# Kernel tuning notes

Measured on AMD Instinct MI355X. Metric: run time of the kernel, lower is better.

Reference implementation:

```python
import jax, jax.numpy as jnp
import numpy as np

EMBED_DIM = 1024
NUM_HEADS = 16
HEAD_DIM = EMBED_DIM // NUM_HEADS


def setup_inputs() -> dict:
    key = jax.random.key(0)
    k_x, k_wqkv, k_bqkv, k_wo, k_bo = jax.random.split(key, 5)
    b, n = 2, 2048
    scale_in = 1.0 / np.sqrt(EMBED_DIM)
    return {
        "x": jax.random.normal(k_x, (b, n, EMBED_DIM), dtype=jnp.float32),
        "W_qkv": jax.random.normal(k_wqkv, (EMBED_DIM, 3 * EMBED_DIM), dtype=jnp.float32) * scale_in,
        "b_qkv": jnp.zeros((3 * EMBED_DIM,), dtype=jnp.float32),
        "W_out": jax.random.normal(k_wo, (EMBED_DIM, EMBED_DIM), dtype=jnp.float32) * scale_in,
        "b_out": jnp.zeros((EMBED_DIM,), dtype=jnp.float32),
    }


def _rope_rotate(t, cos, sin):
    # t: [b, h, n, hd]; cos/sin: [1, 1, n, hd//2]
    t1, t2 = jnp.split(t, 2, axis=-1)
    return jnp.concatenate([cos * t1 - sin * t2, sin * t1 + cos * t2], axis=-1)


def reference(x, W_qkv, b_qkv, W_out, b_out):
    b, n, d = x.shape
    h, hd = NUM_HEADS, HEAD_DIM

    qkv = x @ W_qkv + b_qkv                      # [b, n, 3d]
    q, k, v = jnp.split(qkv, 3, axis=-1)
    q, k, v = [t.reshape(b, n, h, hd).transpose(0, 2, 1, 3) for t in (q, k, v)]

    # RoPE tables
    hd2 = hd // 2
    theta = 10000.0 ** (-2.0 * jnp.arange(hd2, dtype=jnp.float32) / hd)
    freqs = jnp.arange(n, dtype=jnp.float32)[:, None] * theta[None, :]  # [n, hd2]
    cos = jnp.cos(freqs)[None, None]
    sin = jnp.sin(freqs)[None, None]
    q = _rope_rotate(q, cos, sin)
    k = _rope_rotate(k, cos, sin)

    scores = jnp.einsum('bhqd,bhkd->bhqk', q, k) / jnp.sqrt(jnp.float32(hd))
    attn = jax.nn.softmax(scores, axis=-1)       # [b, h, n, n]
    out = jnp.einsum('bhqk,bhkd->bhqd', attn, v)
    out = out.transpose(0, 2, 1, 3).reshape(b, n, d)
    return out @ W_out + b_out
```

## Files before the change

### kernel.cpp

```cpp
#include <hip/hip_runtime.h>
#include <hip/hip_bf16.h>
#include <math.h>

#define EMBED 1024
#define NHEAD 16
#define HD 64
#define BATCH 2
#define SEQ 2048
#define MTOT (BATCH * SEQ)
#define QKVN (3 * EMBED)

typedef __attribute__((ext_vector_type(8))) short short8;
typedef __attribute__((ext_vector_type(4))) float f32x4;

typedef __attribute__((address_space(1))) const unsigned int GUI;
typedef __attribute__((address_space(3))) unsigned int LUI;

__device__ __forceinline__ void gload_lds16(const void* src, void* dst) {
  __builtin_amdgcn_global_load_lds((GUI*)src, (LUI*)dst, 16, 0, 0);
}

__device__ __forceinline__ unsigned short f2bf(float f) {
  unsigned u = __builtin_bit_cast(unsigned, f);
  u += 0x7fffu + ((u >> 16) & 1u);
  return (unsigned short)(u >> 16);
}

__device__ __forceinline__ unsigned cvt_pk_bf16(float lo, float hi) {
  unsigned r;
  asm("v_cvt_pk_bf16_f32 %0, %1, %2" : "=v"(r) : "v"(lo), "v"(hi));
  return r;
}


__global__ __launch_bounds__(256) void k_cvt(const float* __restrict__ in,
                                             unsigned short* __restrict__ out, int n4) {
  int i = blockIdx.x * 256 + threadIdx.x;
  if (i >= n4) return;
  float4 v = reinterpret_cast<const float4*>(in)[i];
  ushort4 o;
  o.x = f2bf(v.x); o.y = f2bf(v.y); o.z = f2bf(v.z); o.w = f2bf(v.w);
  reinterpret_cast<ushort4*>(out)[i] = o;
}

__global__ __launch_bounds__(256) void k_transpose_cvt(const float* __restrict__ W,
                                                       unsigned short* __restrict__ WT,
                                                       int K, int Ncols) {
  __shared__ float tile[32][33];
  int n0 = blockIdx.x * 32, k0 = blockIdx.y * 32;
  int tc = threadIdx.x & 31, tr = threadIdx.x >> 5;
  for (int i = 0; i < 4; i++) {
    int r = tr + i * 8;
    tile[r][tc] = W[(size_t)(k0 + r) * Ncols + n0 + tc];
  }
  __syncthreads();
  for (int i = 0; i < 4; i++) {
    int r = tr + i * 8;
    WT[(size_t)(n0 + r) * K + k0 + tc] = f2bf(tile[tc][r]);
  }
}

__global__ __launch_bounds__(256) void k_rope_tables(float* __restrict__ cosT,
                                                     float* __restrict__ sinT) {
  int idx = blockIdx.x * 256 + threadIdx.x;
  if (idx >= SEQ * 32) return;
  int pos = idx >> 5, i = idx & 31;
  double theta = exp((double)i * -0.28782313662425575);
  double f = (double)pos * theta;
  cosT[idx] = (float)cos(f);
  sinT[idx] = (float)sin(f);
}

__device__ __forceinline__ void gemm_mainloop(const unsigned short* __restrict__ A,
                                              const unsigned short* __restrict__ Bt,
                                              unsigned short* Al, unsigned short* Bl,
                                              size_t m0, size_t n0,
                                              int tid, int l15, int g, int wm, int wn,
                                              f32x4 acc[4][4]) {
  const int w = tid >> 6;
  const int lane = tid & 63;
  const int srow = lane >> 3, slot = lane & 7;
  for (int k0 = 0; k0 < 1024; k0 += 64) {
    __syncthreads();
    for (int it = 0; it < 4; it++) {
      const int r = w * 32 + it * 8 + srow;
      const int sc = (slot ^ (r & 7)) * 8;
      gload_lds16(A + (m0 + r) * 1024 + k0 + sc, &Al[(w * 32 + it * 8) * 64]);
      gload_lds16(Bt + (n0 + r) * 1024 + k0 + sc, &Bl[(w * 32 + it * 8) * 64]);
    }
    __syncthreads();
    for (int kk = 0; kk < 2; kk++) {
      short8 fa[4], fb[4];
      const int xr = ((kk * 4 + g) ^ (l15 & 7)) * 8;
      for (int i = 0; i < 4; i++)
        fa[i] = *reinterpret_cast<const short8*>(&Al[(wm * 64 + i * 16 + l15) * 64 + xr]);
      for (int j = 0; j < 4; j++)
        fb[j] = *reinterpret_cast<const short8*>(&Bl[(wn * 64 + j * 16 + l15) * 64 + xr]);
      for (int i = 0; i < 4; i++)
        for (int j = 0; j < 4; j++)
          acc[i][j] = __builtin_amdgcn_mfma_f32_16x16x32_bf16(fa[i], fb[j], acc[i][j], 0, 0, 0);
    }
  }
}

__global__ __launch_bounds__(256) void k_qkv_gemm(const unsigned short* __restrict__ A,
                                                  const unsigned short* __restrict__ Bt,
                                                  const float* __restrict__ bias,
                                                  const float* __restrict__ cosT,
                                                  const float* __restrict__ sinT,
                                                  unsigned short* __restrict__ Qb,
                                                  unsigned short* __restrict__ Kb,
                                                  unsigned short* __restrict__ Vtg) {
  __shared__ alignas(16) unsigned short Al[128 * 64];
  __shared__ alignas(16) unsigned short Bl[128 * 64];
  const int tid = threadIdx.x;
  const int lane = tid & 63, l15 = lane & 15, g = lane >> 4;
  const int wid = tid >> 6, wm = wid >> 1, wn = wid & 1;
  const size_t m0 = (size_t)blockIdx.y * 128;
  const size_t n0 = (size_t)blockIdx.x * 128;
  f32x4 acc[4][4] = {};
  gemm_mainloop(A, Bt, Al, Bl, m0, n0, tid, l15, g, wm, wn, acc);

  const int cbase = (int)n0 + wn * 64;
  const int sec = cbase >> 10;
  const int head = (cbase & 1023) >> 6;
  float bia[4];
  for (int j = 0; j < 4; j++) bia[j] = bias[cbase + j * 16 + l15];
  const size_t mw = m0 + wm * 64;

  if (sec == 2) {
    for (int i = 0; i < 4; i++)
      for (int r = 0; r < 4; r++) {
        size_t m = mw + i * 16 + g * 4 + r;
        int bb = (int)(m >> 11), pos = (int)(m & 2047);
        size_t hb = (size_t)(bb * NHEAD + head) * HD;
        for (int j = 0; j < 4; j++) {
          int d = j * 16 + l15;
          Vtg[(hb + d) * SEQ + pos] = f2bf(acc[i][j][r] + bia[j]);
        }
      }
  } else {
    unsigned short* dst = sec ? Kb : Qb;
    const float qs = sec ? 1.0f : 0.125f;
    for (int i = 0; i < 4; i++)
      for (int r = 0; r < 4; r++) {
        size_t m = mw + i * 16 + g * 4 + r;
        int bb = (int)(m >> 11), pos = (int)(m & 2047);
        size_t base = ((size_t)(bb * NHEAD + head) * SEQ + pos) * HD;
        const float* cr = cosT + pos * 32;
        const float* sr = sinT + pos * 32;
        for (int pl = 0; pl < 2; pl++) {
          int ii = pl * 16 + l15;
          float c = cr[ii], s = sr[ii];
          float lo = acc[i][pl][r] + bia[pl];
          float hi = acc[i][pl + 2][r] + bia[pl + 2];
          dst[base + ii]      = f2bf((c * lo - s * hi) * qs);
          dst[base + 32 + ii] = f2bf((s * lo + c * hi) * qs);
        }
      }
  }
}

__global__ __launch_bounds__(256) void k_out_gemm(const unsigned short* __restrict__ A,
                                                  const unsigned short* __restrict__ Bt,
                                                  const float* __restrict__ bias,
                                                  float* __restrict__ out) {
  __shared__ alignas(16) unsigned short Al[128 * 64];
  __shared__ alignas(16) unsigned short Bl[128 * 64];
  const int tid = threadIdx.x;
  const int lane = tid & 63, l15 = lane & 15, g = lane >> 4;
  const int wid = tid >> 6, wm = wid >> 1, wn = wid & 1;
  const size_t m0 = (size_t)blockIdx.y * 128;
  const size_t n0 = (size_t)blockIdx.x * 128;
  f32x4 acc[4][4] = {};
  gemm_mainloop(A, Bt, Al, Bl, m0, n0, tid, l15, g, wm, wn, acc);

  const int cbase = (int)n0 + wn * 64;
  const size_t mw = m0 + wm * 64;
  for (int i = 0; i < 4; i++)
    for (int r = 0; r < 4; r++) {
      size_t m = mw + i * 16 + g * 4 + r;
      for (int j = 0; j < 4; j++) {
        int col = cbase + j * 16 + l15;
        out[m * EMBED + col] = acc[i][j][r] + bias[col];
      }
    }
}

__global__ __launch_bounds__(256) void k_attn(const unsigned short* __restrict__ Q,
                                              const unsigned short* __restrict__ Kg,
                                              const unsigned short* __restrict__ Vtg,
                                              unsigned short* __restrict__ AO) {
  __shared__ alignas(16) unsigned short Kt[64 * 64];
  __shared__ alignas(16) unsigned short Vt[64 * 64];
  const int tid = threadIdx.x, w = tid >> 6, lane = tid & 63;
  const int l15 = lane & 15, g = lane >> 4;
  const int srow = lane >> 3, slot = lane & 7;
  const int bh = blockIdx.y;
  const unsigned short* Qp = Q + (size_t)bh * SEQ * HD;
  const unsigned short* Kp = Kg + (size_t)bh * SEQ * HD;
  const unsigned short* Vp = Vtg + (size_t)bh * HD * SEQ;
  const int q0 = blockIdx.x * 64 + w * 16;

  short8 aq[2];
  for (int kk = 0; kk < 2; kk++)
    aq[kk] = *reinterpret_cast<const short8*>(Qp + (size_t)(q0 + l15) * HD + kk * 32 + g * 8);

  f32x4 o[4] = {};
  float mrow = -INFINITY, lrow = 0.f;

  for (int t = 0; t < SEQ / 64; t++) {
    const int kb = t * 64;
    __syncthreads();
    for (int it = 0; it < 2; it++) {
      const int r = w * 16 + it * 8 + srow;
      const int sc = (slot ^ (r & 7)) * 8;
      gload_lds16(Kp + (size_t)(kb + r) * HD + sc, &Kt[(w * 16 + it * 8) * 64]);
      gload_lds16(Vp + (size_t)r * SEQ + kb + sc, &Vt[(w * 16 + it * 8) * 64]);
    }
    __syncthreads();

    f32x4 s[4] = {};
    for (int kk = 0; kk < 2; kk++) {
      const int xr = ((kk * 4 + g) ^ (l15 & 7)) * 8;
      for (int c = 0; c < 4; c++) {
        short8 ak = *reinterpret_cast<const short8*>(&Kt[(c * 16 + l15) * 64 + xr]);
        s[c] = __builtin_amdgcn_mfma_f32_16x16x32_bf16(ak, aq[kk], s[c], 0, 0, 0);
      }
    }

    float tm = s[0][0];
#pragma unroll
    for (int c = 0; c < 4; c++)
#pragma unroll
      for (int r = 0; r < 4; r++) tm = fmaxf(tm, s[c][r]);
    tm = fmaxf(tm, __shfl_xor(tm, 16, 64));
    tm = fmaxf(tm, __shfl_xor(tm, 32, 64));

    if (!__all(tm <= mrow + 8.0f)) {
      float mn = fmaxf(mrow, tm);
      float fac = __expf(mrow - mn);
      lrow *= fac;
#pragma unroll
      for (int c2 = 0; c2 < 4; c2++)
#pragma unroll
        for (int r = 0; r < 4; r++) o[c2][r] *= fac;
      mrow = mn;
    }

    float rs = 0.f;
    unsigned wpk[8];
#pragma unroll
    for (int c = 0; c < 4; c++) {
      float p0 = __expf(s[c][0] - mrow);
      float p1 = __expf(s[c][1] - mrow);
      float p2 = __expf(s[c][2] - mrow);
      float p3 = __expf(s[c][3] - mrow);
      rs += (p0 + p1) + (p2 + p3);
      wpk[2 * c]     = cvt_pk_bf16(p0, p1);
      wpk[2 * c + 1] = cvt_pk_bf16(p2, p3);
    }
    rs += __shfl_xor(rs, 16, 64);
    rs += __shfl_xor(rs, 32, 64);
    lrow += rs;

#pragma unroll
    for (int kk = 0; kk < 2; kk++) {
      short8 pb = __builtin_bit_cast(short8,
          uint4{wpk[4 * kk], wpk[4 * kk + 1], wpk[4 * kk + 2], wpk[4 * kk + 3]});
#pragma unroll
      for (int c2 = 0; c2 < 4; c2++) {
        const unsigned short* vrow = &Vt[(c2 * 16 + l15) * 64];
        const int rx = l15 & 7;
        uint2 v1 = *reinterpret_cast<const uint2*>(vrow + ((4 * kk + (g >> 1)) ^ rx) * 8 + (g & 1) * 4);
        uint2 v2 = *reinterpret_cast<const uint2*>(vrow + ((4 * kk + 2 + (g >> 1)) ^ rx) * 8 + (g & 1) * 4);
        short8 av = __builtin_bit_cast(short8, uint4{v1.x, v1.y, v2.x, v2.y});
        o[c2] = __builtin_amdgcn_mfma_f32_16x16x32_bf16(av, pb, o[c2], 0, 0, 0);
      }
    }
  }

  const int bb = bh >> 4, h = bh & 15;
  const float inv = 1.f / lrow;
  const int pos = q0 + l15;
  unsigned short* dst = AO + ((size_t)bb * SEQ + pos) * EMBED + h * HD;
#pragma unroll
  for (int c2 = 0; c2 < 4; c2++) {
    uint2 pk;
    pk.x = cvt_pk_bf16(o[c2][0] * inv, o[c2][1] * inv);
    pk.y = cvt_pk_bf16(o[c2][2] * inv, o[c2][3] * inv);
    *reinterpret_cast<uint2*>(dst + c2 * 16 + g * 4) = pk;
  }
}

extern "C" void kernel_launch(void* const* d_in, const int* in_sizes, int n_in,
                              void* d_out, int out_size, void* d_ws, size_t ws_size,
                              hipStream_t stream) {
  const float* x    = (const float*)d_in[0];
  const float* Wqkv = (const float*)d_in[1];
  const float* bqkv = (const float*)d_in[2];
  const float* Wout = (const float*)d_in[3];
  const float* bout = (const float*)d_in[4];
  float* out = (float*)d_out;

  char* ws = (char*)d_ws;
  size_t off = 0;
  auto carve = [&](size_t bytes) {
    char* p = ws + off;
    off += (bytes + 255) & ~(size_t)255;
    return p;
  };
  float* cosT           = (float*)carve((size_t)SEQ * 32 * 4);
  float* sinT           = (float*)carve((size_t)SEQ * 32 * 4);
  unsigned short* Xb    = (unsigned short*)carve((size_t)MTOT * EMBED * 2);
  unsigned short* WqkvT = (unsigned short*)carve((size_t)QKVN * EMBED * 2);
  unsigned short* WoT   = (unsigned short*)carve((size_t)EMBED * EMBED * 2);
  unsigned short* Qb    = (unsigned short*)carve((size_t)MTOT * EMBED * 2);
  unsigned short* Kb    = (unsigned short*)carve((size_t)MTOT * EMBED * 2);
  unsigned short* Vtg   = (unsigned short*)carve((size_t)MTOT * EMBED * 2);
  unsigned short* AO    = (unsigned short*)carve((size_t)MTOT * EMBED * 2);

  k_cvt<<<(MTOT * EMBED / 4 + 255) / 256, 256, 0, stream>>>(x, Xb, MTOT * EMBED / 4);
  k_transpose_cvt<<<dim3(QKVN / 32, EMBED / 32), 256, 0, stream>>>(Wqkv, WqkvT, EMBED, QKVN);
  k_transpose_cvt<<<dim3(EMBED / 32, EMBED / 32), 256, 0, stream>>>(Wout, WoT, EMBED, EMBED);
  k_rope_tables<<<(SEQ * 32) / 256, 256, 0, stream>>>(cosT, sinT);

  k_qkv_gemm<<<dim3(QKVN / 128, MTOT / 128), 256, 0, stream>>>(Xb, WqkvT, bqkv, cosT, sinT, Qb, Kb, Vtg);
  k_attn<<<dim3(SEQ / 64, BATCH * NHEAD), 256, 0, stream>>>(Qb, Kb, Vtg, AO);
  k_out_gemm<<<dim3(EMBED / 128, MTOT / 128), 256, 0, stream>>>(AO, WoT, bout, out);
}
```

Measured before the change: 153.8 us.

## Use exp2 softmax, vectorized V store, smaller out-GEMM tiles, setprio

Folds log2(e) into the Q scale so the softmax uses exp2 instead of expf, and raises the lazy-rescale threshold to match. Writes the transposed V tile as packed 4-element stores with an XOR swizzle, and adjusts the V read offsets in attention to agree. Halves the out-GEMM N tile to 64 so the grid has twice as many blocks, wraps the attention MFMA sections in s_setprio, and computes the RoPE tables in float instead of double. The float RoPE tables lose accuracy at large positions, and the V swizzle has to match exactly between writer and reader.

```diff
diff --git a/kernel.cpp b/kernel.cpp
--- a/kernel.cpp
+++ b/kernel.cpp
@@ -31,6 +31,8 @@
   asm("v_cvt_pk_bf16_f32 %0, %1, %2" : "=v"(r) : "v"(lo), "v"(hi));
   return r;
 }
+
+#define QSCALE 0.1803368801111191f
 
 
 __global__ __launch_bounds__(256) void k_cvt(const float* __restrict__ in,
@@ -65,10 +67,10 @@
   int idx = blockIdx.x * 256 + threadIdx.x;
   if (idx >= SEQ * 32) return;
   int pos = idx >> 5, i = idx & 31;
-  double theta = exp((double)i * -0.28782313662425575);
-  double f = (double)pos * theta;
-  cosT[idx] = (float)cos(f);
-  sinT[idx] = (float)sin(f);
+  float theta = __expf((float)i * -0.28782313662425575f);
+  float f = (float)pos * theta;
+  cosT[idx] = cosf(f);
+  sinT[idx] = sinf(f);
 }
 
 __device__ __forceinline__ void gemm_mainloop(const unsigned short* __restrict__ A,
@@ -129,19 +131,22 @@
   const size_t mw = m0 + wm * 64;
 
   if (sec == 2) {
-    for (int i = 0; i < 4; i++)
-      for (int r = 0; r < 4; r++) {
-        size_t m = mw + i * 16 + g * 4 + r;
-        int bb = (int)(m >> 11), pos = (int)(m & 2047);
-        size_t hb = (size_t)(bb * NHEAD + head) * HD;
-        for (int j = 0; j < 4; j++) {
-          int d = j * 16 + l15;
-          Vtg[(hb + d) * SEQ + pos] = f2bf(acc[i][j][r] + bia[j]);
-        }
-      }
+    const int dsw = ((l15 >> 3) & 1) << 2;
+    for (int i = 0; i < 4; i++) {
+      size_t mbase = mw + i * 16 + g * 4;
+      int bb = (int)(mbase >> 11), pos0 = (int)(mbase & 2047);
+      size_t hb = (size_t)(bb * NHEAD + head) * HD;
+      for (int j = 0; j < 4; j++) {
+        int d = j * 16 + l15;
+        uint2 pk;
+        pk.x = cvt_pk_bf16(acc[i][j][0] + bia[j], acc[i][j][1] + bia[j]);
+        pk.y = cvt_pk_bf16(acc[i][j][2] + bia[j], acc[i][j][3] + bia[j]);
+        *reinterpret_cast<uint2*>(Vtg + (hb + d) * SEQ + (pos0 ^ dsw)) = pk;
+      }
+    }
   } else {
     unsigned short* dst = sec ? Kb : Qb;
-    const float qs = sec ? 1.0f : 0.125f;
+    const float qs = sec ? 1.0f : QSCALE;
     for (int i = 0; i < 4; i++)
       for (int r = 0; r < 4; r++) {
         size_t m = mw + i * 16 + g * 4 + r;
@@ -166,21 +171,48 @@
                                                   const float* __restrict__ bias,
                                                   float* __restrict__ out) {
   __shared__ alignas(16) unsigned short Al[128 * 64];
-  __shared__ alignas(16) unsigned short Bl[128 * 64];
+  __shared__ alignas(16) unsigned short Bl[64 * 64];
   const int tid = threadIdx.x;
   const int lane = tid & 63, l15 = lane & 15, g = lane >> 4;
   const int wid = tid >> 6, wm = wid >> 1, wn = wid & 1;
+  const int w = wid;
+  const int srow = lane >> 3, slot = lane & 7;
   const size_t m0 = (size_t)blockIdx.y * 128;
-  const size_t n0 = (size_t)blockIdx.x * 128;
-  f32x4 acc[4][4] = {};
-  gemm_mainloop(A, Bt, Al, Bl, m0, n0, tid, l15, g, wm, wn, acc);
-
-  const int cbase = (int)n0 + wn * 64;
+  const size_t n0 = (size_t)blockIdx.x * 64;
+  f32x4 acc[4][2] = {};
+
+  for (int k0 = 0; k0 < 1024; k0 += 64) {
+    __syncthreads();
+    for (int it = 0; it < 4; it++) {
+      const int r = w * 32 + it * 8 + srow;
+      const int sc = (slot ^ (r & 7)) * 8;
+      gload_lds16(A + (m0 + r) * 1024 + k0 + sc, &Al[(w * 32 + it * 8) * 64]);
+    }
+    for (int it = 0; it < 2; it++) {
+      const int r = w * 16 + it * 8 + srow;
+      const int sc = (slot ^ (r & 7)) * 8;
+      gload_lds16(Bt + (n0 + r) * 1024 + k0 + sc, &Bl[(w * 16 + it * 8) * 64]);
+    }
+    __syncthreads();
+    for (int kk = 0; kk < 2; kk++) {
+      short8 fa[4], fb[2];
+      const int xr = ((kk * 4 + g) ^ (l15 & 7)) * 8;
+      for (int i = 0; i < 4; i++)
+        fa[i] = *reinterpret_cast<const short8*>(&Al[(wm * 64 + i * 16 + l15) * 64 + xr]);
+      for (int j = 0; j < 2; j++)
+        fb[j] = *reinterpret_cast<const short8*>(&Bl[(wn * 32 + j * 16 + l15) * 64 + xr]);
+      for (int i = 0; i < 4; i++)
+        for (int j = 0; j < 2; j++)
+          acc[i][j] = __builtin_amdgcn_mfma_f32_16x16x32_bf16(fa[i], fb[j], acc[i][j], 0, 0, 0);
+    }
+  }
+
+  const int cbase = (int)n0 + wn * 32;
   const size_t mw = m0 + wm * 64;
   for (int i = 0; i < 4; i++)
     for (int r = 0; r < 4; r++) {
       size_t m = mw + i * 16 + g * 4 + r;
-      for (int j = 0; j < 4; j++) {
+      for (int j = 0; j < 2; j++) {
         int col = cbase + j * 16 + l15;
         out[m * EMBED + col] = acc[i][j][r] + bias[col];
       }
@@ -221,6 +253,7 @@
     __syncthreads();
 
     f32x4 s[4] = {};
+    __builtin_amdgcn_s_setprio(1);
     for (int kk = 0; kk < 2; kk++) {
       const int xr = ((kk * 4 + g) ^ (l15 & 7)) * 8;
       for (int c = 0; c < 4; c++) {
@@ -228,6 +261,7 @@
         s[c] = __builtin_amdgcn_mfma_f32_16x16x32_bf16(ak, aq[kk], s[c], 0, 0, 0);
       }
     }
+    __builtin_amdgcn_s_setprio(0);
 
     float tm = s[0][0];
 #pragma unroll
@@ -237,9 +271,9 @@
     tm = fmaxf(tm, __shfl_xor(tm, 16, 64));
     tm = fmaxf(tm, __shfl_xor(tm, 32, 64));
 
-    if (!__all(tm <= mrow + 8.0f)) {
+    if (!__all(tm <= mrow + 11.5f)) {
       float mn = fmaxf(mrow, tm);
-      float fac = __expf(mrow - mn);
+      float fac = __builtin_exp2f(mrow - mn);
       lrow *= fac;
 #pragma unroll
       for (int c2 = 0; c2 < 4; c2++)
@@ -252,10 +286,10 @@
     unsigned wpk[8];
 #pragma unroll
     for (int c = 0; c < 4; c++) {
-      float p0 = __expf(s[c][0] - mrow);
-      float p1 = __expf(s[c][1] - mrow);
-      float p2 = __expf(s[c][2] - mrow);
-      float p3 = __expf(s[c][3] - mrow);
+      float p0 = __builtin_exp2f(s[c][0] - mrow);
+      float p1 = __builtin_exp2f(s[c][1] - mrow);
+      float p2 = __builtin_exp2f(s[c][2] - mrow);
+      float p3 = __builtin_exp2f(s[c][3] - mrow);
       rs += (p0 + p1) + (p2 + p3);
       wpk[2 * c]     = cvt_pk_bf16(p0, p1);
       wpk[2 * c + 1] = cvt_pk_bf16(p2, p3);
@@ -264,6 +298,9 @@
     rs += __shfl_xor(rs, 32, 64);
     lrow += rs;
 
+    const int rx = l15 & 7;
+    const int h4 = ((g ^ (l15 >> 3)) & 1) * 4;
+    __builtin_amdgcn_s_setprio(1);
 #pragma unroll
     for (int kk = 0; kk < 2; kk++) {
       short8 pb = __builtin_bit_cast(short8,
@@ -271,13 +308,13 @@
 #pragma unroll
       for (int c2 = 0; c2 < 4; c2++) {
         const unsigned short* vrow = &Vt[(c2 * 16 + l15) * 64];
-        const int rx = l15 & 7;
-        uint2 v1 = *reinterpret_cast<const uint2*>(vrow + ((4 * kk + (g >> 1)) ^ rx) * 8 + (g & 1) * 4);
-        uint2 v2 = *reinterpret_cast<const uint2*>(vrow + ((4 * kk + 2 + (g >> 1)) ^ rx) * 8 + (g & 1) * 4);
+        uint2 v1 = *reinterpret_cast<const uint2*>(vrow + ((4 * kk + (g >> 1)) ^ rx) * 8 + h4);
+        uint2 v2 = *reinterpret_cast<const uint2*>(vrow + ((4 * kk + 2 + (g >> 1)) ^ rx) * 8 + h4);
         short8 av = __builtin_bit_cast(short8, uint4{v1.x, v1.y, v2.x, v2.y});
         o[c2] = __builtin_amdgcn_mfma_f32_16x16x32_bf16(av, pb, o[c2], 0, 0, 0);
       }
     }
+    __builtin_amdgcn_s_setprio(0);
   }
 
   const int bb = bh >> 4, h = bh & 15;
@@ -327,5 +364,5 @@
 
   k_qkv_gemm<<<dim3(QKVN / 128, MTOT / 128), 256, 0, stream>>>(Xb, WqkvT, bqkv, cosT, sinT, Qb, Kb, Vtg);
   k_attn<<<dim3(SEQ / 64, BATCH * NHEAD), 256, 0, stream>>>(Qb, Kb, Vtg, AO);
-  k_out_gemm<<<dim3(EMBED / 128, MTOT / 128), 256, 0, stream>>>(AO, WoT, bout, out);
-}
+  k_out_gemm<<<dim3(EMBED / 64, MTOT / 128), 256, 0, stream>>>(AO, WoT, bout, out);
+}
```

After: 157.5 us. 1.02x slower.
